# Performance work log

Measured on AMD Instinct MI355X. Metric: run time of the kernel, lower is better.

## Reference

```python
import jax, jax.numpy as jnp
import numpy as np

N_NODES = 100000
N_EDGES = 1600000
F_IN = 128
OUT = 32
PERIODS = 12


def setup_inputs() -> dict:
    key = jax.random.key(0)
    ks = jax.random.split(key, 12)
    s = 0.05
    return {
        'x': jax.random.normal(ks[0], (N_NODES, F_IN, PERIODS), jnp.float32),
        'edge_index': jax.random.randint(ks[1], (2, N_EDGES), 0, N_NODES, dtype=jnp.int64),
        'Wz': jax.random.normal(ks[2], (F_IN, OUT), jnp.float32) * s,
        'bz': jnp.zeros((OUT,), jnp.float32),
        'Lz': jax.random.normal(ks[3], (2 * OUT, OUT), jnp.float32) * s,
        'lbz': jnp.zeros((OUT,), jnp.float32),
        'Wh': jax.random.normal(ks[4], (F_IN, OUT), jnp.float32) * s,
        'bh': jnp.zeros((OUT,), jnp.float32),
        'Lh': jax.random.normal(ks[5], (2 * OUT, OUT), jnp.float32) * s,
        'lbh': jnp.zeros((OUT,), jnp.float32),
        'att': jax.random.normal(ks[6], (PERIODS,), jnp.float32),
        'Wlin': jax.random.normal(ks[7], (OUT, PERIODS), jnp.float32) * s,
        'blin': jnp.zeros((PERIODS,), jnp.float32),
    }


def _gcn_norm(edge_index, n):
    # GCNConv normalization with self loops: D^-1/2 (A+I) D^-1/2
    loop = jnp.arange(n, dtype=edge_index.dtype)
    row = jnp.concatenate([edge_index[0], loop])  # sources
    col = jnp.concatenate([edge_index[1], loop])  # targets
    deg = jax.ops.segment_sum(jnp.ones(row.shape[0], jnp.float32), col, num_segments=n)
    dis = jnp.where(deg > 0, jax.lax.rsqrt(deg), 0.0)
    return row, col, dis[row] * dis[col]


def reference(x, edge_index, Wz, bz, Lz, lbz, Wh, bh, Lh, lbh, att, Wlin, blin):
    n = x.shape[0]
    row, col, norm = _gcn_norm(edge_index, n)
    probs = jax.nn.softmax(att)
    xP = jnp.transpose(x, (2, 0, 1))  # [P, N, F]
    H0 = jnp.zeros((n, OUT), x.dtype)

    def conv(xp, W, b):
        xw = xp @ W                              # [N, OUT]
        msg = xw[row] * norm[:, None]            # gather at source
        return jax.ops.segment_sum(msg, col, num_segments=n) + b

    def step(acc, inp):
        xp, p = inp
        # TGCN cell with H=0 (A3TGCN passes H=None each period)
        Z = jax.nn.sigmoid(jnp.concatenate([conv(xp, Wz, bz), H0], axis=1) @ Lz + lbz)
        Ht = jnp.tanh(jnp.concatenate([conv(xp, Wh, bh), H0], axis=1) @ Lh + lbh)
        Hp = (1.0 - Z) * Ht                      # Z*H + (1-Z)*Ht with H=0
        return acc + p * Hp, None

    acc, _ = jax.lax.scan(step, H0, (xP, probs))
    h = jax.nn.relu(acc)
    return h @ Wlin + blin
```

## Files before the change

kernel.cpp:

```cpp
#include <hip/hip_runtime.h>
#include <hip/hip_fp16.h>

#define N_NODES 100000
#define N_EDGES 1600000
#define F_IN 128
#define OUT 32
#define PERIODS 12

__global__ void k_prep(const float* __restrict__ Wz, const float* __restrict__ bz,
                       const float* __restrict__ Lz, const float* __restrict__ lbz,
                       const float* __restrict__ Wh, const float* __restrict__ bh,
                       const float* __restrict__ Lh, const float* __restrict__ lbh,
                       const float* __restrict__ att,
                       float* __restrict__ M, float* __restrict__ cc,
                       float* __restrict__ probs) {
    int t = threadIdx.x;
    for (int idx = t; idx < F_IN * 64; idx += 256) {
        int f = idx >> 6, c = idx & 63;
        const float* W = (c < 32) ? Wz : Wh;
        const float* L = (c < 32) ? Lz : Lh;
        int cj = c & 31;
        float s = 0.f;
        #pragma unroll 8
        for (int j = 0; j < 32; ++j) s += W[f * 32 + j] * L[j * 32 + cj];
        M[idx] = s;
    }
    if (t < 64) {
        int c = t & 31;
        const float* b  = (t < 32) ? bz : bh;
        const float* L  = (t < 32) ? Lz : Lh;
        const float* lb = (t < 32) ? lbz : lbh;
        float s = lb[c];
        for (int j = 0; j < 32; ++j) s += b[j] * L[j * 32 + c];
        cc[t] = s;
    }
    if (t == 0) {
        float m = att[0];
        for (int p = 1; p < PERIODS; ++p) m = fmaxf(m, att[p]);
        float e[PERIODS]; float sum = 0.f;
        for (int p = 0; p < PERIODS; ++p) { e[p] = expf(att[p] - m); sum += e[p]; }
        for (int p = 0; p < PERIODS; ++p) probs[p] = e[p] / sum;
    }
}

__global__ void k_count(const int* __restrict__ ei, int* __restrict__ cnt) {
    int e = blockIdx.x * 256 + threadIdx.x;
    if (e < N_EDGES) {
        int c = ei[N_EDGES + e];
        if ((unsigned)c < N_NODES) atomicAdd(&cnt[c], 1);
    }
}

__global__ void k_dis(const int* __restrict__ cnt, float* __restrict__ dis) {
    int i = blockIdx.x * 256 + threadIdx.x;
    if (i < N_NODES) dis[i] = rsqrtf((float)(cnt[i] + 1));
}

__global__ void k_scan1(const int* __restrict__ cnt, int* __restrict__ rp,
                        int* __restrict__ partials) {
    __shared__ int s[256];
    int t = threadIdx.x;
    int i = blockIdx.x * 256 + t;
    int v = (i < N_NODES) ? cnt[i] : 0;
    s[t] = v;
    __syncthreads();
    for (int off = 1; off < 256; off <<= 1) {
        int y = (t >= off) ? s[t - off] : 0;
        __syncthreads();
        s[t] += y;
        __syncthreads();
    }
    if (i < N_NODES) rp[i] = s[t] - v;
    if (t == 255) partials[blockIdx.x] = s[255];
}

__global__ void k_scan2(int* __restrict__ partials, int np) {
    __shared__ int s[512];
    int t = threadIdx.x;
    int v = (t < np) ? partials[t] : 0;
    s[t] = v;
    __syncthreads();
    for (int off = 1; off < 512; off <<= 1) {
        int y = (t >= off) ? s[t - off] : 0;
        __syncthreads();
        s[t] += y;
        __syncthreads();
    }
    if (t < np) partials[t] = s[t] - v;
}

__global__ void k_scan3(int* __restrict__ rp, const int* __restrict__ partials) {
    int i = blockIdx.x * 256 + threadIdx.x;
    if (i < N_NODES) rp[i] += partials[blockIdx.x];
    if (i == 0) rp[N_NODES] = N_EDGES;
}

__global__ void k_fill(const int* __restrict__ ei, const int* __restrict__ rp,
                       int* __restrict__ cnt, int* __restrict__ srcIdx) {
    int e = blockIdx.x * 256 + threadIdx.x;
    if (e < N_EDGES) {
        int c = ei[N_EDGES + e];
        int r = ei[e];
        if ((unsigned)c < N_NODES) {
            int pos = rp[c] + atomicSub(&cnt[c], 1) - 1;
            srcIdx[pos] = r;
        }
    }
}

#define XSTR 196
__global__ __launch_bounds__(512, 2) void k_proj5(const float* __restrict__ x,
                                                  const float* __restrict__ M,
                                                  __half* __restrict__ U) {
    __shared__ float sx[64 * XSTR];
    int t = threadIdx.x;
    int L = t & 63;
    int co = __builtin_amdgcn_readfirstlane(t >> 6);
    int nb0 = blockIdx.x * 64;
    int node = nb0 + L;

    const float4* xg = reinterpret_cast<const float4*>(x);

    float acc[8][PERIODS];
    #pragma unroll
    for (int c = 0; c < 8; ++c)
        #pragma unroll
        for (int p = 0; p < PERIODS; ++p) acc[c][p] = 0.f;

    const float* sxL = &sx[L * XSTR];

    for (int kc = 0; kc < 8; ++kc) {
        __syncthreads();
        #pragma unroll
        for (int i = 0; i < 6; ++i) {
            int j = t + 512 * i;
            int g = j / 48;
            int wi = j - g * 48;
            int gsrc = nb0 + g; if (gsrc >= N_NODES) gsrc = N_NODES - 1;
            *reinterpret_cast<float4*>(&sx[g * XSTR + wi * 4]) =
                xg[(size_t)gsrc * 384 + kc * 48 + wi];
        }
        __syncthreads();

        #pragma unroll 4
        for (int fi = 0; fi < 16; ++fi) {
            int f = kc * 16 + fi;
            float4 m0 = *reinterpret_cast<const float4*>(&M[f * 64 + co * 8]);
            float4 m1 = *reinterpret_cast<const float4*>(&M[f * 64 + co * 8 + 4]);
            float4 x0 = *reinterpret_cast<const float4*>(&sxL[fi * 12 + 0]);
            float4 x1 = *reinterpret_cast<const float4*>(&sxL[fi * 12 + 4]);
            float4 x2 = *reinterpret_cast<const float4*>(&sxL[fi * 12 + 8]);
            float mm[8] = {m0.x, m0.y, m0.z, m0.w, m1.x, m1.y, m1.z, m1.w};
            float xv[PERIODS] = {x0.x, x0.y, x0.z, x0.w,
                                 x1.x, x1.y, x1.z, x1.w,
                                 x2.x, x2.y, x2.z, x2.w};
            #pragma unroll
            for (int c = 0; c < 8; ++c)
                #pragma unroll
                for (int p = 0; p < PERIODS; ++p)
                    acc[c][p] = fmaf(mm[c], xv[p], acc[c][p]);
        }
    }

    if (node < N_NODES) {
        __half* un = U + (size_t)node * 768 + co * 8;
        #pragma unroll
        for (int p = 0; p < PERIODS; ++p) {
            union { uint4 u; __half2 h[4]; } r;
            r.h[0] = __floats2half2_rn(acc[0][p], acc[1][p]);
            r.h[1] = __floats2half2_rn(acc[2][p], acc[3][p]);
            r.h[2] = __floats2half2_rn(acc[4][p], acc[5][p]);
            r.h[3] = __floats2half2_rn(acc[6][p], acc[7][p]);
            *reinterpret_cast<uint4*>(un + p * 64) = r.u;
        }
    }
}

__global__ void k_agg(const __half* __restrict__ U, const int* __restrict__ rp,
                      const int* __restrict__ srcIdx, const float* __restrict__ dis,
                      const float* __restrict__ cc, const float* __restrict__ probs,
                      const float* __restrict__ Wlin, const float* __restrict__ blin,
                      float* __restrict__ out) {
    int n = blockIdx.x;
    int t = threadIdx.x;
    float dn = dis[n];

    float a0, a1, a2, a3;
    {
        union { uint2 u; __half2 h[2]; } r;
        r.u = reinterpret_cast<const uint2*>(U + (size_t)n * 768)[t];
        float2 f0 = __half22float2(r.h[0]);
        float2 f1 = __half22float2(r.h[1]);
        float w = dn * dn;
        a0 = w * f0.x; a1 = w * f0.y; a2 = w * f1.x; a3 = w * f1.y;
    }
    int beg = rp[n], end = rp[n + 1];
    int e = beg;
    for (; e + 3 < end; e += 4) {
        int s0 = srcIdx[e], s1 = srcIdx[e + 1], s2 = srcIdx[e + 2], s3 = srcIdx[e + 3];
        float w0 = dis[s0] * dn, w1 = dis[s1] * dn, w2 = dis[s2] * dn, w3 = dis[s3] * dn;
        union { uint2 u; __half2 h[2]; } r0, r1, r2, r3;
        r0.u = reinterpret_cast<const uint2*>(U + (size_t)s0 * 768)[t];
        r1.u = reinterpret_cast<const uint2*>(U + (size_t)s1 * 768)[t];
        r2.u = reinterpret_cast<const uint2*>(U + (size_t)s2 * 768)[t];
        r3.u = reinterpret_cast<const uint2*>(U + (size_t)s3 * 768)[t];
        float2 f0, f1;
        f0 = __half22float2(r0.h[0]); f1 = __half22float2(r0.h[1]);
        a0 += w0 * f0.x; a1 += w0 * f0.y; a2 += w0 * f1.x; a3 += w0 * f1.y;
        f0 = __half22float2(r1.h[0]); f1 = __half22float2(r1.h[1]);
        a0 += w1 * f0.x; a1 += w1 * f0.y; a2 += w1 * f1.x; a3 += w1 * f1.y;
        f0 = __half22float2(r2.h[0]); f1 = __half22float2(r2.h[1]);
        a0 += w2 * f0.x; a1 += w2 * f0.y; a2 += w2 * f1.x; a3 += w2 * f1.y;
        f0 = __half22float2(r3.h[0]); f1 = __half22float2(r3.h[1]);
        a0 += w3 * f0.x; a1 += w3 * f0.y; a2 += w3 * f1.x; a3 += w3 * f1.y;
    }
    for (; e < end; ++e) {
        int s = srcIdx[e];
        float w = dis[s] * dn;
        union { uint2 u; __half2 h[2]; } r;
        r.u = reinterpret_cast<const uint2*>(U + (size_t)s * 768)[t];
        float2 f0 = __half22float2(r.h[0]);
        float2 f1 = __half22float2(r.h[1]);
        a0 += w * f0.x; a1 += w * f0.y; a2 += w * f1.x; a3 += w * f1.y;
    }

    __shared__ float sacc[768];
    __shared__ float sterm[PERIODS * 32];
    __shared__ float shf[32];
    sacc[4 * t + 0] = a0; sacc[4 * t + 1] = a1;
    sacc[4 * t + 2] = a2; sacc[4 * t + 3] = a3;
    __syncthreads();

    for (int w2 = t; w2 < PERIODS * 32; w2 += 192) {
        int p = w2 >> 5, c = w2 & 31;
        float z = sacc[p * 64 + c]      + cc[c];
        float h = sacc[p * 64 + 32 + c] + cc[32 + c];
        float zs = 1.f / (1.f + __expf(-z));
        sterm[w2] = probs[p] * (1.f - zs) * tanhf(h);
    }
    __syncthreads();

    if (t < 32) {
        float s = 0.f;
        #pragma unroll
        for (int p = 0; p < PERIODS; ++p) s += sterm[p * 32 + t];
        shf[t] = fmaxf(s, 0.f);
    }
    __syncthreads();

    if (t < PERIODS) {
        float o = blin[t];
        #pragma unroll 8
        for (int c = 0; c < OUT; ++c) o += shf[c] * Wlin[c * PERIODS + t];
        out[(size_t)n * PERIODS + t] = o;
    }
}

extern "C" void kernel_launch(void* const* d_in, const int* in_sizes, int n_in,
                              void* d_out, int out_size, void* d_ws, size_t ws_size,
                              hipStream_t stream) {
    const float* x    = (const float*)d_in[0];
    const int*   ei   = (const int*)d_in[1];
    const float* Wz   = (const float*)d_in[2];
    const float* bz   = (const float*)d_in[3];
    const float* Lz   = (const float*)d_in[4];
    const float* lbz  = (const float*)d_in[5];
    const float* Wh   = (const float*)d_in[6];
    const float* bh   = (const float*)d_in[7];
    const float* Lh   = (const float*)d_in[8];
    const float* lbh  = (const float*)d_in[9];
    const float* att  = (const float*)d_in[10];
    const float* Wlin = (const float*)d_in[11];
    const float* blin = (const float*)d_in[12];
    float* out = (float*)d_out;

    char* w = (char*)d_ws;
    size_t off = 0;
    __half* U      = (__half*)(w + off); off += (size_t)N_NODES * 768 * 2;
    float*  M      = (float*)(w + off);  off += 128 * 64 * 4;
    float*  cc     = (float*)(w + off);  off += 256;
    float*  probs  = (float*)(w + off);  off += 64;
    float*  dis    = (float*)(w + off);  off += N_NODES * 4;
    int*    cnt    = (int*)(w + off);    off += N_NODES * 4;
    int*    rp     = (int*)(w + off);    off += (N_NODES + 1) * 4 + 12;
    int*    parts  = (int*)(w + off);    off += 2048;
    int*    srcIdx = (int*)(w + off);    off += (size_t)N_EDGES * 4;
    (void)ws_size; (void)in_sizes; (void)n_in; (void)out_size;

    const int SCAN_BLOCKS = (N_NODES + 255) / 256;

    (void)hipMemsetAsync(cnt, 0, N_NODES * 4, stream);

    k_prep<<<1, 256, 0, stream>>>(Wz, bz, Lz, lbz, Wh, bh, Lh, lbh, att, M, cc, probs);
    k_count<<<(N_EDGES + 255) / 256, 256, 0, stream>>>(ei, cnt);
    k_dis<<<SCAN_BLOCKS, 256, 0, stream>>>(cnt, dis);
    k_scan1<<<SCAN_BLOCKS, 256, 0, stream>>>(cnt, rp, parts);
    k_scan2<<<1, 512, 0, stream>>>(parts, SCAN_BLOCKS);
    k_scan3<<<SCAN_BLOCKS, 256, 0, stream>>>(rp, parts);
    k_fill<<<(N_EDGES + 255) / 256, 256, 0, stream>>>(ei, rp, cnt, srcIdx);
    k_proj5<<<(N_NODES + 63) / 64, 512, 0, stream>>>(x, M, U);
    k_agg<<<N_NODES, 192, 0, stream>>>(U, rp, srcIdx, dis, cc, probs, Wlin, blin, out);
}
```

Measured before the change: 998.2 us.

## Double-buffer x tiles in projection kernel with register prefetch

Converts the projection kernel's shared-memory staging to a double-buffered scheme. The next chunk of x is loaded into registers while the current chunk is computed, then stored to the alternate buffer. This removes one barrier per chunk and aims to hide global load latency behind the FMA loop. It doubles LDS use per block and adds prefetch registers, which may reduce occupancy or cause spills.

```diff
diff --git a/kernel.cpp b/kernel.cpp
--- a/kernel.cpp
+++ b/kernel.cpp
@@ -109,10 +109,10 @@
 }
 
 #define XSTR 196
-__global__ __launch_bounds__(512, 2) void k_proj5(const float* __restrict__ x,
+__global__ __launch_bounds__(512, 2) void k_proj6(const float* __restrict__ x,
                                                   const float* __restrict__ M,
                                                   __half* __restrict__ U) {
-    __shared__ float sx[64 * XSTR];
+    __shared__ float sx[2][64 * XSTR];
     int t = threadIdx.x;
     int L = t & 63;
     int co = __builtin_amdgcn_readfirstlane(t >> 6);
@@ -120,6 +120,26 @@
     int node = nb0 + L;
 
     const float4* xg = reinterpret_cast<const float4*>(x);
+
+    int sg[6], swi[6], gsrc[6];
+    #pragma unroll
+    for (int i = 0; i < 6; ++i) {
+        int j = t + 512 * i;
+        int g = j / 48;
+        sg[i] = g;
+        swi[i] = j - g * 48;
+        int s = nb0 + g;
+        gsrc[i] = (s >= N_NODES) ? (N_NODES - 1) : s;
+    }
+
+    float4 st[6];
+    #pragma unroll
+    for (int i = 0; i < 6; ++i)
+        st[i] = xg[(size_t)gsrc[i] * 384 + swi[i]];
+    #pragma unroll
+    for (int i = 0; i < 6; ++i)
+        *reinterpret_cast<float4*>(&sx[0][sg[i] * XSTR + swi[i] * 4]) = st[i];
+    __syncthreads();
 
     float acc[8][PERIODS];
     #pragma unroll
@@ -127,21 +147,14 @@
         #pragma unroll
         for (int p = 0; p < PERIODS; ++p) acc[c][p] = 0.f;
 
-    const float* sxL = &sx[L * XSTR];
-
     for (int kc = 0; kc < 8; ++kc) {
-        __syncthreads();
-        #pragma unroll
-        for (int i = 0; i < 6; ++i) {
-            int j = t + 512 * i;
-            int g = j / 48;
-            int wi = j - g * 48;
-            int gsrc = nb0 + g; if (gsrc >= N_NODES) gsrc = N_NODES - 1;
-            *reinterpret_cast<float4*>(&sx[g * XSTR + wi * 4]) =
-                xg[(size_t)gsrc * 384 + kc * 48 + wi];
-        }
-        __syncthreads();
-
+        int cur = kc & 1;
+        if (kc < 7) {
+            #pragma unroll
+            for (int i = 0; i < 6; ++i)
+                st[i] = xg[(size_t)gsrc[i] * 384 + (kc + 1) * 48 + swi[i]];
+        }
+        const float* sxL = &sx[cur][L * XSTR];
         #pragma unroll 4
         for (int fi = 0; fi < 16; ++fi) {
             int f = kc * 16 + fi;
@@ -160,6 +173,12 @@
                 for (int p = 0; p < PERIODS; ++p)
                     acc[c][p] = fmaf(mm[c], xv[p], acc[c][p]);
         }
+        if (kc < 7) {
+            #pragma unroll
+            for (int i = 0; i < 6; ++i)
+                *reinterpret_cast<float4*>(&sx[cur ^ 1][sg[i] * XSTR + swi[i] * 4]) = st[i];
+        }
+        __syncthreads();
     }
 
     if (node < N_NODES) {
@@ -298,6 +317,6 @@
     k_scan2<<<1, 512, 0, stream>>>(parts, SCAN_BLOCKS);
     k_scan3<<<SCAN_BLOCKS, 256, 0, stream>>>(rp, parts);
     k_fill<<<(N_EDGES + 255) / 256, 256, 0, stream>>>(ei, rp, cnt, srcIdx);
-    k_proj5<<<(N_NODES + 63) / 64, 512, 0, stream>>>(x, M, U);
+    k_proj6<<<(N_NODES + 63) / 64, 512, 0, stream>>>(x, M, U);
     k_agg<<<N_NODES, 192, 0, stream>>>(U, rp, srcIdx, dis, cc, probs, Wlin, blin, out);
 }
```

Measured after the change: 945.5 us. 1.06x faster.
